# Kernel optimization log

Measured on AMD Instinct MI355X. Metric: run time of the kernel, lower is better.

Reference implementation:

```python
import jax, jax.numpy as jnp
import numpy as np

NUM_DIM = 2
N, P, Q, C = 2048, 2048, 64, 2

def _mlp(x, layers, activate_final):
    n = len(layers)
    for i, (w, b) in enumerate(layers):
        x = x @ w + b
        if i < n - 1 or activate_final:
            x = jnp.tanh(x)
    return x

def setup_inputs() -> dict:
    key = jax.random.key(0)
    ks = jax.random.split(key, 24)
    s = 0.3  # param scale for numerical sanity
    return {
        "phase_coords": jax.random.normal(ks[0], (N, 2 * NUM_DIM), jnp.float32),
        "boundary_coords": jax.random.normal(ks[1], (N, 2 * NUM_DIM), jnp.float32),
        "coeff_position": jax.random.normal(ks[2], (P, NUM_DIM), jnp.float32),
        "coeff_values": jax.random.uniform(ks[3], (P, C), jnp.float32),
        "scattering_kernel_coords": jax.random.normal(ks[4], (Q, NUM_DIM), jnp.float32),
        "scattering_kernel": jax.random.uniform(ks[5], (Q,), jnp.float32),
        "velocity_weights": jax.random.uniform(ks[6], (Q,), jnp.float32) / Q,
        "attn_w1": s * jax.random.normal(ks[7], (6, 32), jnp.float32),
        "attn_b1": jnp.zeros((32,), jnp.float32),
        "attn_w2": s * jax.random.normal(ks[8], (32, 32), jnp.float32),
        "attn_b2": jnp.zeros((32,), jnp.float32),
        "attn_w3": s * jax.random.normal(ks[9], (32, 1), jnp.float32),
        "attn_b3": jnp.zeros((1,), jnp.float32),
        "green_w1": s * jax.random.normal(ks[10], (4 * NUM_DIM + C, 64), jnp.float32),
        "green_b1": jnp.zeros((64,), jnp.float32),
        "green_w2": s * jax.random.normal(ks[11], (64, 64), jnp.float32),
        "green_b2": jnp.zeros((64,), jnp.float32),
        "green_w3": s * jax.random.normal(ks[12], (64, 64), jnp.float32),
        "green_b3": jnp.zeros((64,), jnp.float32),
        "res_w": s * jax.random.normal(ks[13], (64, 64), jnp.float32),
        "res_b": jnp.zeros((64,), jnp.float32),
        "final_w": s * jax.random.normal(ks[14], (64, 1), jnp.float32),
        "final_b": jnp.zeros((1,), jnp.float32),
    }

def reference(phase_coords, boundary_coords, coeff_position, coeff_values,
              scattering_kernel_coords, scattering_kernel, velocity_weights,
              attn_w1, attn_b1, attn_w2, attn_b2, attn_w3, attn_b3,
              green_w1, green_b1, green_w2, green_b2, green_w3, green_b3,
              res_w, res_b, final_w, final_b):
    attn_layers = [(attn_w1, attn_b1), (attn_w2, attn_b2), (attn_w3, attn_b3)]
    green_layers = [(green_w1, green_b1), (green_w2, green_b2), (green_w3, green_b3)]

    x, v = phase_coords[:, :NUM_DIM], phase_coords[:, NUM_DIM:]     # (N,2),(N,2)
    xp, vp = boundary_coords[:, :NUM_DIM], boundary_coords[:, NUM_DIM:]

    # --- CoefficientNet: MLP attention logits + geometric mask + softmax over P ---
    ang = v / jnp.sqrt(jnp.sum(v**2, -1, keepdims=True) + 1e-16)     # (N,2)
    rel = x[:, None, :] - coeff_position[None, :, :]                 # (N,P,2)
    dist = jnp.sqrt(jnp.sum(rel**2, -1) + 1e-16)                     # (N,P)
    pos_loc = jnp.einsum('npd,nd->np', rel, ang)                     # (N,P)
    ang_loc = pos_loc / (dist + 1e-8)
    frames = jnp.stack([ang_loc, pos_loc], -1)                       # (N,P,2)
    coords = jnp.concatenate([x, v], -1)                             # (N,4)
    qk = jnp.concatenate(
        [jnp.broadcast_to(coords[:, None, :], (coords.shape[0], frames.shape[1], coords.shape[1])), frames], -1)  # (N,P,6)
    logits = _mlp(qk, attn_layers, False)[..., 0]                    # (N,P)
    logits = jnp.where(pos_loc > 0, logits, -1e30)
    aw = jax.nn.softmax(logits, axis=-1)
    coeff = jnp.exp(-(aw @ coeff_values))                            # (N,C)

    # --- GreenFunctionBlock (coefficients only depend on (x,v)) ---
    g0 = jnp.exp(_mlp(jnp.concatenate([x, v, xp, vp, coeff], -1), green_layers, True))  # (N,64)

    # --- res block depth=1: quadrature over velocity_prime (argnum=3) ---
    w_quad = (1.0 - scattering_kernel) * velocity_weights            # (Q,)
    Nn = x.shape[0]; Qq = scattering_kernel_coords.shape[0]
    base = jnp.concatenate([x, v, xp], -1)                           # (N,6)
    inp_q = jnp.concatenate([
        jnp.broadcast_to(base[:, None, :], (Nn, Qq, base.shape[1])),
        jnp.broadcast_to(scattering_kernel_coords[None, :, :], (Nn, Qq, NUM_DIM)),
        jnp.broadcast_to(coeff[:, None, :], (Nn, Qq, coeff.shape[1])),
    ], -1)                                                           # (N,Q,10)
    gq = jnp.exp(_mlp(inp_q, green_layers, True))                    # (N,Q,64)
    quad = jnp.einsum('nqh,q->nh', gq, w_quad)                       # (N,64)
    res = jnp.tanh(quad @ res_w + res_b)                             # widths[-1:], activate_final
    out = g0 + res
    return out @ final_w + final_b                                   # (N,1)
```

## Files before the change

### kernel.cpp

```cpp
#include <hip/hip_runtime.h>

#define NN 2048
#define PP 2048
#define QQ 64
#define GR_ROWS 4
#define GR_SLOTS 80
#define GR_MT 5

typedef __attribute__((ext_vector_type(8))) short short8;
typedef __attribute__((ext_vector_type(4))) float f32x4;
typedef __attribute__((ext_vector_type(4))) unsigned u32x4;

union V4 { u32x4 u; short8 s; };

#if __has_builtin(__builtin_amdgcn_exp2f)
#define EXP2(x) __builtin_amdgcn_exp2f(x)
#else
#define EXP2(x) exp2f(x)
#endif

__device__ __forceinline__ float fast_rcp(float x) { return __builtin_amdgcn_rcpf(x); }

__device__ __forceinline__ float fast_tanh(float x) {
    float t = EXP2(x * 2.885390082f);
    return 1.0f - 2.0f * __builtin_amdgcn_rcpf(t + 1.0f);
}

__device__ __forceinline__ unsigned cvt_pk_bf16(float lo, float hi) {
    unsigned r;
    asm("v_cvt_pk_bf16_f32 %0, %1, %2" : "=v"(r) : "v"(lo), "v"(hi));
    return r;
}
__device__ __forceinline__ unsigned short bf16_bits(float f) {
    unsigned u = __builtin_bit_cast(unsigned, f);
    u += 0x7FFFu + ((u >> 16) & 1u);
    return (unsigned short)(u >> 16);
}

__global__ __launch_bounds__(128) void attn_logits_kernel(
    const float* __restrict__ pc, const float* __restrict__ cp,
    const float* __restrict__ w1, const float* __restrict__ b1,
    const float* __restrict__ w2, const float* __restrict__ b2,
    const float* __restrict__ w3, const float* __restrict__ b3,
    float* __restrict__ logits_g)
{
    __shared__ float2 sap[2][256];
    __shared__ unsigned short sidx[2][256];

    const int t = threadIdx.x;
    const int w = t >> 6, lane = t & 63;
    const int c15 = lane & 15, kg = lane >> 4;
    const int k0 = kg * 8;
    const int n  = blockIdx.x >> 2;
    const int p0 = (blockIdx.x & 3) * 512 + w * 256;

    const float b3v = b3[0];
    const float x0 = pc[n*4+0], x1 = pc[n*4+1];
    const float v0 = pc[n*4+2], v1 = pc[n*4+3];
    const float rinv = __builtin_amdgcn_rsqf(v0*v0 + v1*v1 + 1e-16f);
    const float a0 = v0 * rinv, a1 = v1 * rinv;

    float* __restrict__ lrow = logits_g + (size_t)n * PP;

    int cnt = 0;
    #pragma unroll
    for (int i = 0; i < 4; ++i) {
        const int p = p0 + i*64 + lane;
        const float2 cpp = ((const float2*)cp)[p];
        const float r0 = x0 - cpp.x;
        const float r1 = x1 - cpp.y;
        const float pos = fmaf(r0, a0, r1*a1);
        const bool f = pos > 0.0f;
        if (!f) lrow[p] = -1e30f;
        const unsigned long long mask = __ballot(f);
        if (f) {
            const int idx = cnt + __popcll(mask & ((1ull << lane) - 1ull));
            const float dist = sqrtf(r0*r0 + r1*r1 + 1e-16f);
            const float angl = pos * fast_rcp(dist + 1e-8f);
            sap[w][idx]  = make_float2(angl, pos);
            sidx[w][idx] = (unsigned short)p;
        }
        cnt += __popcll(mask);
    }

    union BF { short8 s8; unsigned u[4]; } B0, B1;
    #pragma unroll
    for (int j2 = 0; j2 < 4; ++j2) {
        const int ka = k0 + 2*j2, kb = ka + 1;
        B0.u[j2] = cvt_pk_bf16(w2[ka*32 + c15],      w2[kb*32 + c15]);
        B1.u[j2] = cvt_pk_bf16(w2[ka*32 + c15 + 16], w2[kb*32 + c15 + 16]);
    }
    float b2a[4], b2b[4], w3a[4], w3b[4];
    #pragma unroll
    for (int r = 0; r < 4; ++r) {
        b2a[r] = b2[kg*4 + r];      b2b[r] = b2[16 + kg*4 + r];
        w3a[r] = w3[kg*4 + r];      w3b[r] = w3[16 + kg*4 + r];
    }
    float cfrag[8], w1a[8], w1b[8];
    #pragma unroll
    for (int j = 0; j < 8; ++j) {
        const int k = k0 + j;
        float c = b1[k];
        c = fmaf(x0, w1[0*32+k], c);
        c = fmaf(x1, w1[1*32+k], c);
        c = fmaf(v0, w1[2*32+k], c);
        c = fmaf(v1, w1[3*32+k], c);
        cfrag[j] = c;
        w1a[j] = w1[4*32+k];
        w1b[j] = w1[5*32+k];
    }

    const int nt = (cnt + 15) >> 4;
    #pragma unroll 2
    for (int tile = 0; tile < nt; ++tile) {
        const int li = tile*16 + c15;
        const float2 ap = sap[w][li < cnt ? li : 0];
        const float angl = ap.x, pos = ap.y;

        union AF { short8 s8; unsigned u[4]; } H;
        #pragma unroll
        for (int j2 = 0; j2 < 4; ++j2) {
            const float ha = fast_tanh(fmaf(angl, w1a[2*j2+0], fmaf(pos, w1b[2*j2+0], cfrag[2*j2+0])));
            const float hb = fast_tanh(fmaf(angl, w1a[2*j2+1], fmaf(pos, w1b[2*j2+1], cfrag[2*j2+1])));
            H.u[j2] = cvt_pk_bf16(ha, hb);
        }

        f32x4 acca = {b2a[0], b2a[1], b2a[2], b2a[3]};
        f32x4 accb = {b2b[0], b2b[1], b2b[2], b2b[3]};
        acca = __builtin_amdgcn_mfma_f32_16x16x32_bf16(B0.s8, H.s8, acca, 0, 0, 0);
        accb = __builtin_amdgcn_mfma_f32_16x16x32_bf16(B1.s8, H.s8, accb, 0, 0, 0);

        float lg = 0.0f;
        #pragma unroll
        for (int r = 0; r < 4; ++r) {
            lg = fmaf(fast_tanh(acca[r]), w3a[r], lg);
            lg = fmaf(fast_tanh(accb[r]), w3b[r], lg);
        }
        lg += __shfl_xor(lg, 16);
        lg += __shfl_xor(lg, 32);

        if (kg == 0 && li < cnt) lrow[sidx[w][li]] = lg + b3v;
    }
}

__global__ __launch_bounds__(256) void attn_softmax_kernel(
    const float* __restrict__ logits_g, const float* __restrict__ cv,
    float* __restrict__ coeff_out)
{
    __shared__ float sred[16];
    const int n = blockIdx.x;
    const int t = threadIdx.x;
    const int wid = t >> 6, lane = t & 63;
    const float* __restrict__ lrow = logits_g + (size_t)n * PP;

    float m = -3.4e38f;
    float lg[PP/256];
    #pragma unroll
    for (int i = 0; i < PP/256; ++i) {
        lg[i] = lrow[i*256 + t];
        m = fmaxf(m, lg[i]);
    }
    #pragma unroll
    for (int off = 32; off; off >>= 1) m = fmaxf(m, __shfl_xor(m, off));
    if (lane == 0) sred[wid] = m;
    __syncthreads();
    m = fmaxf(fmaxf(sred[0], sred[1]), fmaxf(sred[2], sred[3]));

    float s = 0.0f, q0 = 0.0f, q1 = 0.0f;
    #pragma unroll
    for (int i = 0; i < PP/256; ++i) {
        const float e = EXP2((lg[i] - m) * 1.44269504f);
        const float2 cvv = ((const float2*)cv)[i*256 + t];
        s += e;
        q0 = fmaf(e, cvv.x, q0);
        q1 = fmaf(e, cvv.y, q1);
    }
    #pragma unroll
    for (int off = 32; off; off >>= 1) {
        s  += __shfl_xor(s, off);
        q0 += __shfl_xor(q0, off);
        q1 += __shfl_xor(q1, off);
    }
    __syncthreads();
    if (lane == 0) {
        sred[4 + wid*3 + 0] = s;
        sred[4 + wid*3 + 1] = q0;
        sred[4 + wid*3 + 2] = q1;
    }
    __syncthreads();
    if (t == 0) {
        float S = 0.0f, Q0 = 0.0f, Q1 = 0.0f;
        #pragma unroll
        for (int w = 0; w < 4; ++w) {
            S  += sred[4 + w*3 + 0];
            Q0 += sred[4 + w*3 + 1];
            Q1 += sred[4 + w*3 + 2];
        }
        const float invS = fast_rcp(S);
        coeff_out[n*2+0] = __expf(-Q0 * invS);
        coeff_out[n*2+1] = __expf(-Q1 * invS);
    }
}

__global__ __launch_bounds__(256) void attn_kernel(
    const float* __restrict__ pc, const float* __restrict__ cp,
    const float* __restrict__ cv,
    const float* __restrict__ w1, const float* __restrict__ b1,
    const float* __restrict__ w2, const float* __restrict__ b2,
    const float* __restrict__ w3, const float* __restrict__ b3,
    float* __restrict__ coeff_out)
{
    __shared__ float2 scpc[PP];
    __shared__ unsigned short slist[PP];
    __shared__ float sred[16];
    __shared__ int scount;

    const int n = blockIdx.x;
    const int t = threadIdx.x;
    const int wid  = t >> 6;
    const int lane = t & 63;
    const int c15  = lane & 15;
    const int kg   = lane >> 4;
    const int k0   = kg * 8;

    const float b3v = b3[0];

    if (t == 0) scount = 0;

    const float x0 = pc[n*4+0], x1 = pc[n*4+1];
    const float v0 = pc[n*4+2], v1 = pc[n*4+3];
    const float rinv = __builtin_amdgcn_rsqf(v0*v0 + v1*v1 + 1e-16f);
    const float a0 = v0 * rinv, a1 = v1 * rinv;

    union BF { short8 s8; unsigned u[4]; } B0, B1;
    #pragma unroll
    for (int j2 = 0; j2 < 4; ++j2) {
        const int ka = k0 + 2*j2, kb = ka + 1;
        B0.u[j2] = cvt_pk_bf16(w2[ka*32 + c15],      w2[kb*32 + c15]);
        B1.u[j2] = cvt_pk_bf16(w2[ka*32 + c15 + 16], w2[kb*32 + c15 + 16]);
    }
    float b2a[4], b2b[4], w3a[4], w3b[4];
    #pragma unroll
    for (int r = 0; r < 4; ++r) {
        b2a[r] = b2[kg*4 + r];      b2b[r] = b2[16 + kg*4 + r];
        w3a[r] = w3[kg*4 + r];      w3b[r] = w3[16 + kg*4 + r];
    }
    float cfrag[8], w1a[8], w1b[8];
    #pragma unroll
    for (int j = 0; j < 8; ++j) {
        const int k = k0 + j;
        float c = b1[k];
        c = fmaf(x0, w1[0*32+k], c);
        c = fmaf(x1, w1[1*32+k], c);
        c = fmaf(v0, w1[2*32+k], c);
        c = fmaf(v1, w1[3*32+k], c);
        cfrag[j] = c;
        w1a[j] = w1[4*32+k];
        w1b[j] = w1[5*32+k];
    }
    __syncthreads();

    #pragma unroll 1
    for (int i = 0; i < PP/256; ++i) {
        const int p = i*256 + t;
        const float2 cpp = ((const float2*)cp)[p];
        const float r0 = x0 - cpp.x;
        const float r1 = x1 - cpp.y;
        const float pos = fmaf(r0, a0, r1*a1);
        const bool f = pos > 0.0f;
        const unsigned long long mask = __ballot(f);
        int base = 0;
        if (lane == 0 && mask) base = atomicAdd(&scount, __popcll(mask));
        base = __shfl(base, 0);
        if (f) {
            const int idx = base + __popcll(mask & ((1ull << lane) - 1ull));
            const float dist = sqrtf(r0*r0 + r1*r1 + 1e-16f);
            const float angl = pos * fast_rcp(dist + 1e-8f);
            slist[idx] = (unsigned short)p;
            scpc[idx] = make_float2(angl, pos);
        }
    }
    __syncthreads();
    const int M  = scount;
    const int Mt = (M + 15) >> 4;

    #pragma unroll 2
    for (int tile = wid; tile < Mt; tile += 4) {
        const int li = tile*16 + c15;
        const float2 ap = scpc[li < M ? li : 0];
        const float angl = ap.x, pos = ap.y;

        union AF { short8 s8; unsigned u[4]; } H;
        #pragma unroll
        for (int j2 = 0; j2 < 4; ++j2) {
            const float ha = fast_tanh(fmaf(angl, w1a[2*j2+0], fmaf(pos, w1b[2*j2+0], cfrag[2*j2+0])));
            const float hb = fast_tanh(fmaf(angl, w1a[2*j2+1], fmaf(pos, w1b[2*j2+1], cfrag[2*j2+1])));
            H.u[j2] = cvt_pk_bf16(ha, hb);
        }

        f32x4 acca = {b2a[0], b2a[1], b2a[2], b2a[3]};
        f32x4 accb = {b2b[0], b2b[1], b2b[2], b2b[3]};
        acca = __builtin_amdgcn_mfma_f32_16x16x32_bf16(B0.s8, H.s8, acca, 0, 0, 0);
        accb = __builtin_amdgcn_mfma_f32_16x16x32_bf16(B1.s8, H.s8, accb, 0, 0, 0);

        float lg = 0.0f;
        #pragma unroll
        for (int r = 0; r < 4; ++r) {
            lg = fmaf(fast_tanh(acca[r]), w3a[r], lg);
            lg = fmaf(fast_tanh(accb[r]), w3b[r], lg);
        }
        lg += __shfl_xor(lg, 16);
        lg += __shfl_xor(lg, 32);

        if (kg == 0 && li < M) scpc[li].x = lg + b3v;
    }
    __syncthreads();

    float m = -3.4e38f;
    if (M > 0)
        for (int i = t; i < M; i += 256) m = fmaxf(m, scpc[i].x);
    #pragma unroll
    for (int off = 32; off; off >>= 1) m = fmaxf(m, __shfl_xor(m, off));
    if (lane == 0) sred[wid] = m;
    __syncthreads();
    m = fmaxf(fmaxf(sred[0], sred[1]), fmaxf(sred[2], sred[3]));

    float s = 0.0f, q0 = 0.0f, q1 = 0.0f;
    if (M > 0) {
        #pragma unroll 2
        for (int i = t; i < M; i += 256) {
            const float e = EXP2((scpc[i].x - m) * 1.44269504f);
            const float2 cvv = ((const float2*)cv)[slist[i]];
            s += e;
            q0 = fmaf(e, cvv.x, q0);
            q1 = fmaf(e, cvv.y, q1);
        }
    } else {
        for (int i = t; i < PP; i += 256) {
            const float2 cvv = ((const float2*)cv)[i];
            s += 1.0f; q0 += cvv.x; q1 += cvv.y;
        }
    }
    #pragma unroll
    for (int off = 32; off; off >>= 1) {
        s  += __shfl_xor(s, off);
        q0 += __shfl_xor(q0, off);
        q1 += __shfl_xor(q1, off);
    }
    __syncthreads();
    if (lane == 0) {
        sred[4 + wid*3 + 0] = s;
        sred[4 + wid*3 + 1] = q0;
        sred[4 + wid*3 + 2] = q1;
    }
    __syncthreads();
    if (t == 0) {
        float S = 0.0f, Q0 = 0.0f, Q1 = 0.0f;
        #pragma unroll
        for (int w = 0; w < 4; ++w) {
            S  += sred[4 + w*3 + 0];
            Q0 += sred[4 + w*3 + 1];
            Q1 += sred[4 + w*3 + 2];
        }
        const float invS = fast_rcp(S);
        coeff_out[n*2+0] = __expf(-Q0 * invS);
        coeff_out[n*2+1] = __expf(-Q1 * invS);
    }
}

__global__ __launch_bounds__(256) void green_kernel(
    const float* __restrict__ pc,  const float* __restrict__ bc,
    const float* __restrict__ skc, const float* __restrict__ sk,
    const float* __restrict__ vw,
    const float* __restrict__ gw1, const float* __restrict__ gb1,
    const float* __restrict__ gw2, const float* __restrict__ gb2,
    const float* __restrict__ gw3, const float* __restrict__ gb3,
    const float* __restrict__ rw,  const float* __restrict__ rb,
    const float* __restrict__ fw,  const float* __restrict__ fb,
    const float* __restrict__ coeff,
    float* __restrict__ out)
{
    __shared__ unsigned short sinA[GR_ROWS*GR_SLOTS*16];
    __shared__ unsigned short shb[4][16*64];
    __shared__ float swq[GR_SLOTS];
    __shared__ float sg0[4][64];
    __shared__ float squad[4][64];

    const int t = threadIdx.x;
    const int w = t >> 6, lane = t & 63;
    const int c15 = lane & 15, kg = lane >> 4;
    const int n0 = blockIdx.x * GR_ROWS;

    V4 Bw1[4], Bw2[2][4], Bw3[2][4];
    #pragma unroll
    for (int nt = 0; nt < 4; ++nt) {
        const int col = c15 + nt*16;
        #pragma unroll
        for (int j2 = 0; j2 < 4; ++j2) {
            const int ka = kg*8 + 2*j2, kb = ka + 1;
            const float va = (ka < 10) ? gw1[ka*64 + col] : 0.0f;
            const float vb = (kb < 10) ? gw1[kb*64 + col] : 0.0f;
            Bw1[nt].u[j2] = cvt_pk_bf16(va, vb);
        }
        #pragma unroll
        for (int kt = 0; kt < 2; ++kt) {
            #pragma unroll
            for (int j2 = 0; j2 < 4; ++j2) {
                const int ka = kt*32 + kg*8 + 2*j2, kb = ka + 1;
                Bw2[kt][nt].u[j2] = cvt_pk_bf16(gw2[ka*64 + col], gw2[kb*64 + col]);
                Bw3[kt][nt].u[j2] = cvt_pk_bf16(gw3[ka*64 + col], gw3[kb*64 + col]);
            }
        }
    }
    float b1c[4], b2c[4], b3c[4];
    #pragma unroll
    for (int nt = 0; nt < 4; ++nt) {
        b1c[nt] = gb1[c15 + nt*16];
        b2c[nt] = gb2[c15 + nt*16];
        b3c[nt] = gb3[c15 + nt*16];
    }

    for (int row = t; row < GR_ROWS*GR_SLOTS; row += 256) {
        const int nl = row / GR_SLOTS;
        const int s  = row - nl*GR_SLOTS;
        const int n  = n0 + nl;
        u32x4 lo = {0u,0u,0u,0u}, hi = {0u,0u,0u,0u};
        if (s <= 64) {
            const float X0 = pc[n*4+0], X1 = pc[n*4+1];
            const float V0 = pc[n*4+2], V1 = pc[n*4+3];
            const float XP0 = bc[n*4+0], XP1 = bc[n*4+1];
            float I6, I7;
            if (s == 64) { I6 = bc[n*4+2]; I7 = bc[n*4+3]; }
            else         { I6 = skc[s*2+0]; I7 = skc[s*2+1]; }
            const float C0 = coeff[n*2+0], C1 = coeff[n*2+1];
            lo[0] = cvt_pk_bf16(X0, X1);
            lo[1] = cvt_pk_bf16(V0, V1);
            lo[2] = cvt_pk_bf16(XP0, XP1);
            lo[3] = cvt_pk_bf16(I6, I7);
            hi[0] = cvt_pk_bf16(C0, C1);
        }
        ((u32x4*)sinA)[row*2 + 0] = lo;
        ((u32x4*)sinA)[row*2 + 1] = hi;
    }
    if (t < GR_SLOTS)
        swq[t] = (t < QQ) ? (1.0f - sk[t]) * vw[t] : 0.0f;
    __syncthreads();

    unsigned short* hb = &shb[w][0];
    float qacc[4] = {0.f, 0.f, 0.f, 0.f};

    #pragma unroll 1
    for (int T = 0; T < GR_MT; ++T) {
        const int rm = w*GR_SLOTS + T*16 + c15;
        V4 A1; A1.u = (u32x4){0u,0u,0u,0u};
        if (kg < 2) A1.u = ((u32x4*)sinA)[rm*2 + kg];

        f32x4 acc1[4];
        #pragma unroll
        for (int nt = 0; nt < 4; ++nt) {
            f32x4 a = {b1c[nt], b1c[nt], b1c[nt], b1c[nt]};
            acc1[nt] = __builtin_amdgcn_mfma_f32_16x16x32_bf16(A1.s, Bw1[nt].s, a, 0, 0, 0);
        }
        #pragma unroll
        for (int nt = 0; nt < 4; ++nt) {
            #pragma unroll
            for (int r = 0; r < 4; ++r) {
                const int rl = kg*4 + r;
                hb[rl*64 + ((c15 + nt*16) ^ ((rl&7)<<3))] = bf16_bits(fast_tanh(acc1[nt][r]));
            }
        }
        V4 A2[2];
        #pragma unroll
        for (int kt = 0; kt < 2; ++kt)
            A2[kt].u = ((u32x4*)hb)[(c15*64 + ((kt*32 + kg*8) ^ ((c15&7)<<3))) >> 3];
        f32x4 acc2[4];
        #pragma unroll
        for (int nt = 0; nt < 4; ++nt) {
            f32x4 a = {b2c[nt], b2c[nt], b2c[nt], b2c[nt]};
            a = __builtin_amdgcn_mfma_f32_16x16x32_bf16(A2[0].s, Bw2[0][nt].s, a, 0, 0, 0);
            acc2[nt] = __builtin_amdgcn_mfma_f32_16x16x32_bf16(A2[1].s, Bw2[1][nt].s, a, 0, 0, 0);
        }
        #pragma unroll
        for (int nt = 0; nt < 4; ++nt) {
            #pragma unroll
            for (int r = 0; r < 4; ++r) {
                const int rl = kg*4 + r;
                hb[rl*64 + ((c15 + nt*16) ^ ((rl&7)<<3))] = bf16_bits(fast_tanh(acc2[nt][r]));
            }
        }
        V4 A3[2];
        #pragma unroll
        for (int kt = 0; kt < 2; ++kt)
            A3[kt].u = ((u32x4*)hb)[(c15*64 + ((kt*32 + kg*8) ^ ((c15&7)<<3))) >> 3];
        f32x4 acc3[4];
        #pragma unroll
        for (int nt = 0; nt < 4; ++nt) {
            f32x4 a = {b3c[nt], b3c[nt], b3c[nt], b3c[nt]};
            a = __builtin_amdgcn_mfma_f32_16x16x32_bf16(A3[0].s, Bw3[0][nt].s, a, 0, 0, 0);
            acc3[nt] = __builtin_amdgcn_mfma_f32_16x16x32_bf16(A3[1].s, Bw3[1][nt].s, a, 0, 0, 0);
        }
        #pragma unroll
        for (int r = 0; r < 4; ++r) {
            const int s = T*16 + kg*4 + r;
            const float wq = swq[s];
            #pragma unroll
            for (int nt = 0; nt < 4; ++nt) {
                const float g = __expf(fast_tanh(acc3[nt][r]));
                qacc[nt] = fmaf(wq, g, qacc[nt]);
                if (T == GR_MT-1 && kg == 0 && r == 0) sg0[w][c15 + nt*16] = g;
            }
        }
    }

    #pragma unroll
    for (int nt = 0; nt < 4; ++nt) {
        qacc[nt] += __shfl_xor(qacc[nt], 16);
        qacc[nt] += __shfl_xor(qacc[nt], 32);
    }
    if (kg == 0) {
        #pragma unroll
        for (int nt = 0; nt < 4; ++nt) squad[w][c15 + nt*16] = qacc[nt];
    }

    const int k = lane;
    float r0a = rb[k], r1a = 0.f, r2a = 0.f, r3a = 0.f;
    #pragma unroll
    for (int j = 0; j < 64; j += 4) {
        const float4 qd = *(const float4*)&squad[w][j];
        r0a = fmaf(qd.x, rw[(j+0)*64 + k], r0a);
        r1a = fmaf(qd.y, rw[(j+1)*64 + k], r1a);
        r2a = fmaf(qd.z, rw[(j+2)*64 + k], r2a);
        r3a = fmaf(qd.w, rw[(j+3)*64 + k], r3a);
    }
    const float resv = fast_tanh((r0a + r1a) + (r2a + r3a));
    float term = (sg0[w][k] + resv) * fw[k];
    #pragma unroll
    for (int off = 32; off; off >>= 1) term += __shfl_xor(term, off);
    if (lane == 0) out[n0 + w] = term + fb[0];
}

extern "C" void kernel_launch(void* const* d_in, const int* in_sizes, int n_in,
                              void* d_out, int out_size, void* d_ws, size_t ws_size,
                              hipStream_t stream) {
    const float* pc  = (const float*)d_in[0];
    const float* bc  = (const float*)d_in[1];
    const float* cp  = (const float*)d_in[2];
    const float* cv  = (const float*)d_in[3];
    const float* skc = (const float*)d_in[4];
    const float* sk  = (const float*)d_in[5];
    const float* vw  = (const float*)d_in[6];
    const float* aw1 = (const float*)d_in[7];
    const float* ab1 = (const float*)d_in[8];
    const float* aw2 = (const float*)d_in[9];
    const float* ab2 = (const float*)d_in[10];
    const float* aw3 = (const float*)d_in[11];
    const float* ab3 = (const float*)d_in[12];
    const float* gw1 = (const float*)d_in[13];
    const float* gb1 = (const float*)d_in[14];
    const float* gw2 = (const float*)d_in[15];
    const float* gb2 = (const float*)d_in[16];
    const float* gw3 = (const float*)d_in[17];
    const float* gb3 = (const float*)d_in[18];
    const float* rw  = (const float*)d_in[19];
    const float* rb  = (const float*)d_in[20];
    const float* fw  = (const float*)d_in[21];
    const float* fb  = (const float*)d_in[22];

    float* coeff = (float*)d_ws;
    float* outp  = (float*)d_out;

    const size_t need = (size_t)NN*2*sizeof(float) + (size_t)NN*PP*sizeof(float);
    if (ws_size >= need) {
        float* logits = (float*)((char*)d_ws + (size_t)NN*2*sizeof(float));
        attn_logits_kernel<<<NN*4, 128, 0, stream>>>(pc, cp, aw1, ab1, aw2, ab2, aw3, ab3,
                                                     logits);
        attn_softmax_kernel<<<NN, 256, 0, stream>>>(logits, cv, coeff);
    } else {
        attn_kernel<<<NN, 256, 0, stream>>>(pc, cp, cv, aw1, ab1, aw2, ab2, aw3, ab3, coeff);
    }
    green_kernel<<<NN/GR_ROWS, 256, 0, stream>>>(pc, bc, skc, sk, vw,
                                                 gw1, gb1, gw2, gb2, gw3, gb3,
                                                 rw, rb, fw, fb, coeff, outp);
}
```

Baseline: 84.98 us.

## Fuse softmax into attention logits kernel using a static max bound and rational tanh

Removes the 16 MB logits buffer and its separate softmax pass. The logits kernel now accumulates exp-weighted partial sums per 256-point chunk, using a static upper bound on the logit (from |b3| + sum|w3|) in place of the row max. A small kernel reduces the eight partials per row, with a fallback when every point is masked. Exp-based tanh is replaced by a clamped Padé approximation that shares one reciprocal across four values, which changes accuracy slightly and risks underflow if the bound is loose.

```diff
diff --git a/kernel.cpp b/kernel.cpp
--- a/kernel.cpp
+++ b/kernel.cpp
@@ -26,6 +26,26 @@
     return 1.0f - 2.0f * __builtin_amdgcn_rcpf(t + 1.0f);
 }
 
+__device__ __forceinline__ void tanh4(const float x0, const float x1,
+                                      const float x2, const float x3,
+                                      float* __restrict__ h) {
+    float n[4], d[4];
+    const float xs[4] = {x0, x1, x2, x3};
+    #pragma unroll
+    for (int j = 0; j < 4; ++j) {
+        const float xc = fminf(fmaxf(xs[j], -4.0f), 4.0f);
+        const float u = xc * xc;
+        n[j] = fmaf(u + 105.0f, u, 945.0f) * xc;
+        d[j] = fmaf(fmaf(15.0f, u, 420.0f), u, 945.0f);
+    }
+    const float p1 = d[0]*d[1], p2 = p1*d[2], p3 = p2*d[3];
+    const float R  = fast_rcp(p3);
+    const float i3 = R*p2,  R2 = R*d[3];
+    const float i2 = R2*p1, R1 = R2*d[2];
+    const float i1 = R1*d[0], i0 = R1*d[1];
+    h[0] = n[0]*i0; h[1] = n[1]*i1; h[2] = n[2]*i2; h[3] = n[3]*i3;
+}
+
 __device__ __forceinline__ unsigned cvt_pk_bf16(float lo, float hi) {
     unsigned r;
     asm("v_cvt_pk_bf16_f32 %0, %1, %2" : "=v"(r) : "v"(lo), "v"(hi));
@@ -39,10 +59,11 @@
 
 __global__ __launch_bounds__(128) void attn_logits_kernel(
     const float* __restrict__ pc, const float* __restrict__ cp,
+    const float* __restrict__ cv,
     const float* __restrict__ w1, const float* __restrict__ b1,
     const float* __restrict__ w2, const float* __restrict__ b2,
     const float* __restrict__ w3, const float* __restrict__ b3,
-    float* __restrict__ logits_g)
+    float4* __restrict__ partials)
 {
     __shared__ float2 sap[2][256];
     __shared__ unsigned short sidx[2][256];
@@ -52,15 +73,14 @@
     const int c15 = lane & 15, kg = lane >> 4;
     const int k0 = kg * 8;
     const int n  = blockIdx.x >> 2;
-    const int p0 = (blockIdx.x & 3) * 512 + w * 256;
+    const int chunk = (blockIdx.x & 3) * 2 + w;
+    const int p0 = chunk * 256;
 
     const float b3v = b3[0];
     const float x0 = pc[n*4+0], x1 = pc[n*4+1];
     const float v0 = pc[n*4+2], v1 = pc[n*4+3];
     const float rinv = __builtin_amdgcn_rsqf(v0*v0 + v1*v1 + 1e-16f);
     const float a0 = v0 * rinv, a1 = v1 * rinv;
-
-    float* __restrict__ lrow = logits_g + (size_t)n * PP;
 
     int cnt = 0;
     #pragma unroll
@@ -71,7 +91,6 @@
         const float r1 = x1 - cpp.y;
         const float pos = fmaf(r0, a0, r1*a1);
         const bool f = pos > 0.0f;
-        if (!f) lrow[p] = -1e30f;
         const unsigned long long mask = __ballot(f);
         if (f) {
             const int idx = cnt + __popcll(mask & ((1ull << lane) - 1ull));
@@ -109,7 +128,13 @@
         w1a[j] = w1[4*32+k];
         w1b[j] = w1[5*32+k];
     }
-
+    float sw3 = 0.0f;
+    #pragma unroll
+    for (int j = 0; j < 32; ++j) sw3 += fabsf(w3[j]);
+    const float Lb = fabsf(b3v) + 1.005f * sw3;
+    const float C_E = (b3v - Lb) * 1.44269504f;
+
+    float s = 0.0f, q0 = 0.0f, q1 = 0.0f;
     const int nt = (cnt + 15) >> 4;
     #pragma unroll 2
     for (int tile = 0; tile < nt; ++tile) {
@@ -117,89 +142,74 @@
         const float2 ap = sap[w][li < cnt ? li : 0];
         const float angl = ap.x, pos = ap.y;
 
+        float pre[8], h[8];
+        #pragma unroll
+        for (int j = 0; j < 8; ++j)
+            pre[j] = fmaf(angl, w1a[j], fmaf(pos, w1b[j], cfrag[j]));
+        tanh4(pre[0], pre[1], pre[2], pre[3], &h[0]);
+        tanh4(pre[4], pre[5], pre[6], pre[7], &h[4]);
+
         union AF { short8 s8; unsigned u[4]; } H;
         #pragma unroll
-        for (int j2 = 0; j2 < 4; ++j2) {
-            const float ha = fast_tanh(fmaf(angl, w1a[2*j2+0], fmaf(pos, w1b[2*j2+0], cfrag[2*j2+0])));
-            const float hb = fast_tanh(fmaf(angl, w1a[2*j2+1], fmaf(pos, w1b[2*j2+1], cfrag[2*j2+1])));
-            H.u[j2] = cvt_pk_bf16(ha, hb);
-        }
+        for (int j2 = 0; j2 < 4; ++j2)
+            H.u[j2] = cvt_pk_bf16(h[2*j2], h[2*j2+1]);
 
         f32x4 acca = {b2a[0], b2a[1], b2a[2], b2a[3]};
         f32x4 accb = {b2b[0], b2b[1], b2b[2], b2b[3]};
         acca = __builtin_amdgcn_mfma_f32_16x16x32_bf16(B0.s8, H.s8, acca, 0, 0, 0);
         accb = __builtin_amdgcn_mfma_f32_16x16x32_bf16(B1.s8, H.s8, accb, 0, 0, 0);
 
+        float ha[4], hb[4];
+        tanh4(acca[0], acca[1], acca[2], acca[3], ha);
+        tanh4(accb[0], accb[1], accb[2], accb[3], hb);
+
         float lg = 0.0f;
         #pragma unroll
         for (int r = 0; r < 4; ++r) {
-            lg = fmaf(fast_tanh(acca[r]), w3a[r], lg);
-            lg = fmaf(fast_tanh(accb[r]), w3b[r], lg);
+            lg = fmaf(ha[r], w3a[r], lg);
+            lg = fmaf(hb[r], w3b[r], lg);
         }
         lg += __shfl_xor(lg, 16);
         lg += __shfl_xor(lg, 32);
 
-        if (kg == 0 && li < cnt) lrow[sidx[w][li]] = lg + b3v;
-    }
-}
-
-__global__ __launch_bounds__(256) void attn_softmax_kernel(
-    const float* __restrict__ logits_g, const float* __restrict__ cv,
-    float* __restrict__ coeff_out)
-{
-    __shared__ float sred[16];
-    const int n = blockIdx.x;
-    const int t = threadIdx.x;
-    const int wid = t >> 6, lane = t & 63;
-    const float* __restrict__ lrow = logits_g + (size_t)n * PP;
-
-    float m = -3.4e38f;
-    float lg[PP/256];
-    #pragma unroll
-    for (int i = 0; i < PP/256; ++i) {
-        lg[i] = lrow[i*256 + t];
-        m = fmaxf(m, lg[i]);
-    }
-    #pragma unroll
-    for (int off = 32; off; off >>= 1) m = fmaxf(m, __shfl_xor(m, off));
-    if (lane == 0) sred[wid] = m;
-    __syncthreads();
-    m = fmaxf(fmaxf(sred[0], sred[1]), fmaxf(sred[2], sred[3]));
-
-    float s = 0.0f, q0 = 0.0f, q1 = 0.0f;
-    #pragma unroll
-    for (int i = 0; i < PP/256; ++i) {
-        const float e = EXP2((lg[i] - m) * 1.44269504f);
-        const float2 cvv = ((const float2*)cv)[i*256 + t];
+        const bool val = (kg == 0) && (li < cnt);
+        const int pidx = val ? (int)sidx[w][li] : 0;
+        const float2 cvv = ((const float2*)cv)[pidx];
+        const float e = val ? EXP2(fmaf(lg, 1.44269504f, C_E)) : 0.0f;
         s += e;
         q0 = fmaf(e, cvv.x, q0);
         q1 = fmaf(e, cvv.y, q1);
     }
-    #pragma unroll
-    for (int off = 32; off; off >>= 1) {
+
+    #pragma unroll
+    for (int off = 1; off < 64; off <<= 1) {
         s  += __shfl_xor(s, off);
         q0 += __shfl_xor(q0, off);
         q1 += __shfl_xor(q1, off);
     }
-    __syncthreads();
-    if (lane == 0) {
-        sred[4 + wid*3 + 0] = s;
-        sred[4 + wid*3 + 1] = q0;
-        sred[4 + wid*3 + 2] = q1;
-    }
-    __syncthreads();
-    if (t == 0) {
-        float S = 0.0f, Q0 = 0.0f, Q1 = 0.0f;
-        #pragma unroll
-        for (int w = 0; w < 4; ++w) {
-            S  += sred[4 + w*3 + 0];
-            Q0 += sred[4 + w*3 + 1];
-            Q1 += sred[4 + w*3 + 2];
-        }
-        const float invS = fast_rcp(S);
-        coeff_out[n*2+0] = __expf(-Q0 * invS);
-        coeff_out[n*2+1] = __expf(-Q1 * invS);
-    }
+    if (lane == 0) partials[n*8 + chunk] = make_float4(s, q0, q1, 0.0f);
+}
+
+__global__ __launch_bounds__(256) void attn_coeff_kernel(
+    const float4* __restrict__ partials, const float* __restrict__ cv,
+    float* __restrict__ coeff_out)
+{
+    const int n = blockIdx.x * 256 + threadIdx.x;
+    float S = 0.0f, Q0 = 0.0f, Q1 = 0.0f;
+    #pragma unroll
+    for (int c = 0; c < 8; ++c) {
+        const float4 P = partials[n*8 + c];
+        S += P.x; Q0 += P.y; Q1 += P.z;
+    }
+    if (!(S > 0.0f)) {
+        S = (float)PP; Q0 = 0.0f; Q1 = 0.0f;
+        for (int p = 0; p < PP; ++p) {
+            Q0 += cv[2*p]; Q1 += cv[2*p+1];
+        }
+    }
+    const float invS = fast_rcp(S);
+    coeff_out[n*2+0] = __expf(-Q0 * invS);
+    coeff_out[n*2+1] = __expf(-Q1 * invS);
 }
 
 __global__ __launch_bounds__(256) void attn_kernel(
@@ -569,12 +579,12 @@
     float* coeff = (float*)d_ws;
     float* outp  = (float*)d_out;
 
-    const size_t need = (size_t)NN*2*sizeof(float) + (size_t)NN*PP*sizeof(float);
+    const size_t need = (size_t)NN*2*sizeof(float) + (size_t)NN*8*sizeof(float4);
     if (ws_size >= need) {
-        float* logits = (float*)((char*)d_ws + (size_t)NN*2*sizeof(float));
-        attn_logits_kernel<<<NN*4, 128, 0, stream>>>(pc, cp, aw1, ab1, aw2, ab2, aw3, ab3,
-                                                     logits);
-        attn_softmax_kernel<<<NN, 256, 0, stream>>>(logits, cv, coeff);
+        float4* partials = (float4*)((char*)d_ws + (size_t)NN*2*sizeof(float));
+        attn_logits_kernel<<<NN*4, 128, 0, stream>>>(pc, cp, cv, aw1, ab1, aw2, ab2,
+                                                     aw3, ab3, partials);
+        attn_coeff_kernel<<<NN/256, 256, 0, stream>>>(partials, cv, coeff);
     } else {
         attn_kernel<<<NN, 256, 0, stream>>>(pc, cp, cv, aw1, ab1, aw2, ab2, aw3, ab3, coeff);
     }
```

After: 111.3 us. 31.0% more time.
